# Optimization experiments

Measured on AMD Instinct MI355X. Metric: run time of the kernel, lower is better.

Reference implementation:

```python
import jax, jax.numpy as jnp
import numpy as np

B, E, D = 4096, 64, 1024

def setup_inputs() -> dict:
    key = jax.random.key(0)
    k1, k2 = jax.random.split(key)
    z = jax.random.normal(k1, (B, D), dtype=jnp.float32)
    expert_keys = jax.random.normal(k2, (E, D), dtype=jnp.float32)
    log_sigma = jnp.zeros((D,), dtype=jnp.float32)
    return {"z": z, "expert_keys": expert_keys, "log_sigma": log_sigma}

def reference(z, expert_keys, log_sigma):
    # diag(sigma_inv) @ diff followed by (. * diff).sum(-1) is exactly an
    # elementwise-scaled squared distance: sum_d exp(-log_sigma_d) * diff_d^2
    sigma_inv = jnp.exp(-log_sigma)                              # [D]
    diff = z[:, None, :] - expert_keys[None, :, :]               # [B, E, D]
    mahalanobis_dist = jnp.einsum('bed,d,bed->be', diff, sigma_inv, diff)  # [B, E]
    similarity = 1.0 / (1.0 + mahalanobis_dist)                  # [B, E]
    weights = jax.nn.softmax(similarity, axis=-1)                # [B, E]
    weighted_expert = weights @ expert_keys                      # [B, D]
    return (similarity, weighted_expert)
```

## Files before the change

kernel.cpp:

```cpp
#include <hip/hip_runtime.h>
#include <hip/hip_bf16.h>

#define B_N 4096
#define E_N 64
#define D_N 1024
#define ROWS 8

typedef __bf16 bf16x8 __attribute__((ext_vector_type(8)));
typedef __bf16 bf16x4 __attribute__((ext_vector_type(4)));
typedef float f32x4 __attribute__((ext_vector_type(4)));


__global__ __launch_bounds__(256) void prep_kernel(
    const float* __restrict__ keys, const float* __restrict__ lsig,
    float* __restrict__ sinv, float* __restrict__ ak,
    __bf16* __restrict__ sk, __bf16* __restrict__ kT)
{
  __shared__ float red[4];
  __shared__ __bf16 tl[64][72];
  const int bid = blockIdx.x;
  const int t = threadIdx.x;

  if (bid < 64) {
    const int e = bid;
    const float4 k4 = *(const float4*)(keys + e * D_N + 4 * t);
    const float4 l4 = *(const float4*)(lsig + 4 * t);
    float4 s4;
    s4.x = expf(-l4.x); s4.y = expf(-l4.y); s4.z = expf(-l4.z); s4.w = expf(-l4.w);
    if (e == 0) *(float4*)(sinv + 4 * t) = s4;
    const float4 sk4 = make_float4(s4.x * k4.x, s4.y * k4.y, s4.z * k4.z, s4.w * k4.w);
    bf16x4 skb;
    skb[0] = (__bf16)sk4.x; skb[1] = (__bf16)sk4.y; skb[2] = (__bf16)sk4.z; skb[3] = (__bf16)sk4.w;
    *(bf16x4*)(sk + e * D_N + 4 * t) = skb;
    float p = sk4.x * k4.x + sk4.y * k4.y + sk4.z * k4.z + sk4.w * k4.w;
    #pragma unroll
    for (int off = 32; off > 0; off >>= 1) p += __shfl_down(p, off);
    if ((t & 63) == 0) red[t >> 6] = p;
    __syncthreads();
    if (t == 0) ak[e] = red[0] + red[1] + red[2] + red[3];
  } else {
    const int d0 = (bid - 64) * 64;
    #pragma unroll
    for (int p = 0; p < 4; ++p) {
      const int e  = p * 16 + (t >> 4);
      const int dd = (t & 15) * 4;
      const float4 k4 = *(const float4*)(keys + (size_t)e * D_N + d0 + dd);
      tl[dd + 0][e] = (__bf16)k4.x; tl[dd + 1][e] = (__bf16)k4.y;
      tl[dd + 2][e] = (__bf16)k4.z; tl[dd + 3][e] = (__bf16)k4.w;
    }
    __syncthreads();
    #pragma unroll
    for (int p = 0; p < 2; ++p) {
      const int dd = p * 32 + (t >> 3);
      const int l8 = t & 7;
      const bf16x8 v = *(const bf16x8*)&tl[dd][l8 * 8];
      *(bf16x8*)(kT + (size_t)(d0 + dd) * E_N + l8 * 8) = v;
    }
  }
}

__global__ __launch_bounds__(256) void main_kernel(
    const float* __restrict__ z, const float* __restrict__ sinv,
    const float* __restrict__ ak, const __bf16* __restrict__ sk,
    const __bf16* __restrict__ kT,
    float* __restrict__ out_sim, float* __restrict__ out_we)
{
  constexpr int ZS = D_N + 8;
  __shared__ __bf16 zlds[ROWS * ZS];
  __shared__ float azs[ROWS];
  __shared__ float simb[ROWS][68];
  __shared__ __bf16 wlds[ROWS][72];
  __shared__ float estage[4][ROWS][64];

  const int t  = threadIdx.x;
  const int b0 = blockIdx.x * ROWS;

  const int sr = t >> 5;
  const int sc = t & 31;
  const float* zrow = z + (size_t)(b0 + sr) * D_N;
  float az = 0.f;
  #pragma unroll
  for (int l = 0; l < 8; ++l) {
    const int c = sc * 4 + l * 128;
    const float4 z4 = *(const float4*)(zrow + c);
    const float4 s4 = *(const float4*)(sinv + c);
    az += s4.x * z4.x * z4.x + s4.y * z4.y * z4.y + s4.z * z4.z * z4.z + s4.w * z4.w * z4.w;
    bf16x4 zb;
    zb[0] = (__bf16)z4.x; zb[1] = (__bf16)z4.y; zb[2] = (__bf16)z4.z; zb[3] = (__bf16)z4.w;
    *(bf16x4*)(&zlds[sr * ZS + c]) = zb;
  }
  az += __shfl_down(az, 16); az += __shfl_down(az, 8);
  az += __shfl_down(az, 4);  az += __shfl_down(az, 2);
  az += __shfl_down(az, 1);
  if (sc == 0) azs[sr] = az;
  __syncthreads();

  const int wave = t >> 6;
  const int lane = t & 63;
  const int ln = lane & 15;
  const int q  = lane >> 4;

  f32x4 acc = {0.f, 0.f, 0.f, 0.f};
  const __bf16* bp = sk + (size_t)(wave * 16 + ln) * D_N + q * 8;
  const __bf16* ap = &zlds[(ln & 7) * ZS + q * 8];
  #pragma unroll 8
  for (int ks = 0; ks < 32; ++ks) {
    const bf16x8 bfr = *(const bf16x8*)(bp + ks * 32);
    const bf16x8 afr = *(const bf16x8*)(ap + ks * 32);
    acc = __builtin_amdgcn_mfma_f32_16x16x32_bf16(afr, bfr, acc, 0, 0, 0);
  }
  const float akv = ak[wave * 16 + ln];
  if (q < 2) {
    #pragma unroll
    for (int i = 0; i < 4; ++i) {
      const int row = q * 4 + i;
      const float dist = azs[row] + akv - 2.0f * acc[i];
      simb[row][wave * 16 + ln] = 1.0f / (1.0f + dist);
    }
  }
  __syncthreads();

  if (t < 32) {
    const int row = t >> 2, seg = t & 3;
    float v[16];
    #pragma unroll
    for (int i = 0; i < 16; ++i) v[i] = simb[row][seg * 16 + i];
    float mx = v[0];
    #pragma unroll
    for (int i = 1; i < 16; ++i) mx = fmaxf(mx, v[i]);
    mx = fmaxf(mx, __shfl_xor(mx, 1));
    mx = fmaxf(mx, __shfl_xor(mx, 2));
    float sum = 0.f;
    #pragma unroll
    for (int i = 0; i < 16; ++i) { v[i] = __expf(v[i] - mx); sum += v[i]; }
    sum += __shfl_xor(sum, 1);
    sum += __shfl_xor(sum, 2);
    const float inv = 1.0f / sum;
    #pragma unroll
    for (int i = 0; i < 16; ++i) wlds[row][seg * 16 + i] = (__bf16)(v[i] * inv);
  }
  __syncthreads();

  if (t < 128) {
    const float4 sv = *(const float4*)&simb[t >> 4][(t & 15) * 4];
    *(float4*)(out_sim + (size_t)(b0 + (t >> 4)) * E_N + (t & 15) * 4) = sv;
  }

  const bf16x8 a0 = *(const bf16x8*)&wlds[ln & 7][q * 8];
  const bf16x8 a1 = *(const bf16x8*)&wlds[ln & 7][32 + q * 8];
  #pragma unroll
  for (int g = 0; g < 4; ++g) {
    #pragma unroll
    for (int i2 = 0; i2 < 4; ++i2) {
      const int dt = wave * 16 + g * 4 + i2;
      const int d0 = dt * 16;
      const __bf16* kp = kT + (size_t)(d0 + ln) * E_N + q * 8;
      const bf16x8 b0f = *(const bf16x8*)(kp);
      const bf16x8 b1f = *(const bf16x8*)(kp + 32);
      f32x4 o = {0.f, 0.f, 0.f, 0.f};
      o = __builtin_amdgcn_mfma_f32_16x16x32_bf16(a0, b0f, o, 0, 0, 0);
      o = __builtin_amdgcn_mfma_f32_16x16x32_bf16(a1, b1f, o, 0, 0, 0);
      if (q < 2) {
        #pragma unroll
        for (int j = 0; j < 4; ++j)
          estage[wave][q * 4 + j][i2 * 16 + ln] = o[j];
      }
    }
    __builtin_amdgcn_wave_barrier();
    #pragma unroll
    for (int j2 = 0; j2 < 2; ++j2) {
      const int f = j2 * 256 + lane * 4;
      const int row = f >> 6, col = f & 63;
      const float4 v = *(const float4*)&estage[wave][row][col];
      *(float4*)(out_we + (size_t)(b0 + row) * D_N + wave * 256 + g * 64 + col) = v;
    }
    __builtin_amdgcn_wave_barrier();
  }
}

extern "C" void kernel_launch(void* const* d_in, const int* in_sizes, int n_in,
                              void* d_out, int out_size, void* d_ws, size_t ws_size,
                              hipStream_t stream)
{
  const float* z    = (const float*)d_in[0];
  const float* keys = (const float*)d_in[1];
  const float* ls   = (const float*)d_in[2];
  float* out_sim = (float*)d_out;
  float* out_we  = out_sim + (size_t)B_N * E_N;
  char* ws = (char*)d_ws;
  float*  sinv = (float*)(ws);
  float*  ak   = (float*)(ws + 4096);
  __bf16* sk   = (__bf16*)(ws + 4352);
  __bf16* kT   = (__bf16*)(ws + 135424);
  prep_kernel<<<80, 256, 0, stream>>>(keys, ls, sinv, ak, sk, kT);
  main_kernel<<<B_N / ROWS, 256, 0, stream>>>(z, sinv, ak, sk, kT, out_sim, out_we);
}
```

Before: 89.13 us.

## Process 16 rows per block to fill MFMA tiles and store outputs directly

Doubles rows per block from 8 to 16 so the 16x16 MFMA tiles are fully used instead of half-wasted, halving the grid size and the per-row re-reads of the scaled keys. The LDS staging buffer for the weighted-expert output is dropped; each lane writes its MFMA results straight to global memory, with d-tiles interleaved across waves. The first kT fragment is prefetched before the barrier. In exchange, the direct scalar stores give only 16 contiguous floats per row and may coalesce worse than the former float4 staged writes, and the grid drops to 256 blocks.

```diff
diff --git a/kernel.cpp b/kernel.cpp
--- a/kernel.cpp
+++ b/kernel.cpp
@@ -4,7 +4,7 @@
 #define B_N 4096
 #define E_N 64
 #define D_N 1024
-#define ROWS 8
+#define ROWS 16
 
 typedef __bf16 bf16x8 __attribute__((ext_vector_type(8)));
 typedef __bf16 bf16x4 __attribute__((ext_vector_type(4)));
@@ -70,18 +70,17 @@
   __shared__ float azs[ROWS];
   __shared__ float simb[ROWS][68];
   __shared__ __bf16 wlds[ROWS][72];
-  __shared__ float estage[4][ROWS][64];
 
   const int t  = threadIdx.x;
   const int b0 = blockIdx.x * ROWS;
 
-  const int sr = t >> 5;
-  const int sc = t & 31;
+  const int sr = t >> 4;
+  const int sc = t & 15;
   const float* zrow = z + (size_t)(b0 + sr) * D_N;
   float az = 0.f;
   #pragma unroll
-  for (int l = 0; l < 8; ++l) {
-    const int c = sc * 4 + l * 128;
+  for (int l = 0; l < 16; ++l) {
+    const int c = sc * 4 + l * 64;
     const float4 z4 = *(const float4*)(zrow + c);
     const float4 s4 = *(const float4*)(sinv + c);
     az += s4.x * z4.x * z4.x + s4.y * z4.y * z4.y + s4.z * z4.z * z4.z + s4.w * z4.w * z4.w;
@@ -89,9 +88,8 @@
     zb[0] = (__bf16)z4.x; zb[1] = (__bf16)z4.y; zb[2] = (__bf16)z4.z; zb[3] = (__bf16)z4.w;
     *(bf16x4*)(&zlds[sr * ZS + c]) = zb;
   }
-  az += __shfl_down(az, 16); az += __shfl_down(az, 8);
-  az += __shfl_down(az, 4);  az += __shfl_down(az, 2);
-  az += __shfl_down(az, 1);
+  az += __shfl_xor(az, 1); az += __shfl_xor(az, 2);
+  az += __shfl_xor(az, 4); az += __shfl_xor(az, 8);
   if (sc == 0) azs[sr] = az;
   __syncthreads();
 
@@ -100,27 +98,31 @@
   const int ln = lane & 15;
   const int q  = lane >> 4;
 
+  const float akv = ak[wave * 16 + ln];
   f32x4 acc = {0.f, 0.f, 0.f, 0.f};
   const __bf16* bp = sk + (size_t)(wave * 16 + ln) * D_N + q * 8;
-  const __bf16* ap = &zlds[(ln & 7) * ZS + q * 8];
+  const __bf16* ap = &zlds[ln * ZS + q * 8];
   #pragma unroll 8
   for (int ks = 0; ks < 32; ++ks) {
     const bf16x8 bfr = *(const bf16x8*)(bp + ks * 32);
     const bf16x8 afr = *(const bf16x8*)(ap + ks * 32);
     acc = __builtin_amdgcn_mfma_f32_16x16x32_bf16(afr, bfr, acc, 0, 0, 0);
   }
-  const float akv = ak[wave * 16 + ln];
-  if (q < 2) {
-    #pragma unroll
-    for (int i = 0; i < 4; ++i) {
-      const int row = q * 4 + i;
-      const float dist = azs[row] + akv - 2.0f * acc[i];
-      simb[row][wave * 16 + ln] = 1.0f / (1.0f + dist);
-    }
+
+  #pragma unroll
+  for (int i = 0; i < 4; ++i) {
+    const int row = q * 4 + i;
+    const float dist = azs[row] + akv - 2.0f * acc[i];
+    simb[row][wave * 16 + ln] = 1.0f / (1.0f + dist);
   }
+
+  const __bf16* kp0 = kT + (size_t)(wave * 16 + ln) * E_N + q * 8;
+  const bf16x8 pb0 = *(const bf16x8*)(kp0);
+  const bf16x8 pb1 = *(const bf16x8*)(kp0 + 32);
+
   __syncthreads();
 
-  if (t < 32) {
+  if (t < 64) {
     const int row = t >> 2, seg = t & 3;
     float v[16];
     #pragma unroll
@@ -141,40 +143,30 @@
   }
   __syncthreads();
 
-  if (t < 128) {
+  {
     const float4 sv = *(const float4*)&simb[t >> 4][(t & 15) * 4];
     *(float4*)(out_sim + (size_t)(b0 + (t >> 4)) * E_N + (t & 15) * 4) = sv;
   }
 
-  const bf16x8 a0 = *(const bf16x8*)&wlds[ln & 7][q * 8];
-  const bf16x8 a1 = *(const bf16x8*)&wlds[ln & 7][32 + q * 8];
+  const bf16x8 a0 = *(const bf16x8*)&wlds[ln][q * 8];
+  const bf16x8 a1 = *(const bf16x8*)&wlds[ln][32 + q * 8];
   #pragma unroll
-  for (int g = 0; g < 4; ++g) {
+  for (int i = 0; i < 16; ++i) {
+    const int dt = wave + 4 * i;
+    const int d0 = dt * 16;
+    bf16x8 b0f, b1f;
+    if (i == 0) { b0f = pb0; b1f = pb1; }
+    else {
+      const __bf16* kp = kT + (size_t)(d0 + ln) * E_N + q * 8;
+      b0f = *(const bf16x8*)(kp);
+      b1f = *(const bf16x8*)(kp + 32);
+    }
+    f32x4 o = {0.f, 0.f, 0.f, 0.f};
+    o = __builtin_amdgcn_mfma_f32_16x16x32_bf16(a0, b0f, o, 0, 0, 0);
+    o = __builtin_amdgcn_mfma_f32_16x16x32_bf16(a1, b1f, o, 0, 0, 0);
     #pragma unroll
-    for (int i2 = 0; i2 < 4; ++i2) {
-      const int dt = wave * 16 + g * 4 + i2;
-      const int d0 = dt * 16;
-      const __bf16* kp = kT + (size_t)(d0 + ln) * E_N + q * 8;
-      const bf16x8 b0f = *(const bf16x8*)(kp);
-      const bf16x8 b1f = *(const bf16x8*)(kp + 32);
-      f32x4 o = {0.f, 0.f, 0.f, 0.f};
-      o = __builtin_amdgcn_mfma_f32_16x16x32_bf16(a0, b0f, o, 0, 0, 0);
-      o = __builtin_amdgcn_mfma_f32_16x16x32_bf16(a1, b1f, o, 0, 0, 0);
-      if (q < 2) {
-        #pragma unroll
-        for (int j = 0; j < 4; ++j)
-          estage[wave][q * 4 + j][i2 * 16 + ln] = o[j];
-      }
-    }
-    __builtin_amdgcn_wave_barrier();
-    #pragma unroll
-    for (int j2 = 0; j2 < 2; ++j2) {
-      const int f = j2 * 256 + lane * 4;
-      const int row = f >> 6, col = f & 63;
-      const float4 v = *(const float4*)&estage[wave][row][col];
-      *(float4*)(out_we + (size_t)(b0 + row) * D_N + wave * 256 + g * 64 + col) = v;
-    }
-    __builtin_amdgcn_wave_barrier();
+    for (int j = 0; j < 4; ++j)
+      out_we[(size_t)(b0 + q * 4 + j) * D_N + d0 + ln] = o[j];
   }
 }
 
```

New measurement: 83.55 us. 1.07x faster.
